# Kernel tuning notes

Measured on AMD Instinct MI355X. Metric: run time of the kernel, lower is better.

The kernel has to match this reference:

```python
import jax, jax.numpy as jnp
import numpy as np

B, T, C = 4, 2048, 1024
H = 16
D = C // H  # head_dim = 64


def setup_inputs() -> dict:
    key = jax.random.key(0)
    k1, k2, k3, k4, k5 = jax.random.split(key, 5)
    s = 1.0 / np.sqrt(C)
    return {
        "x": jax.random.normal(k1, (B, T, C), dtype=jnp.float32),
        "Wqkv": jax.random.normal(k2, (C, 3 * C), dtype=jnp.float32) * s,
        "bqkv": jax.random.normal(k3, (3 * C,), dtype=jnp.float32) * 0.02,
        "Wproj": jax.random.normal(k4, (C, C), dtype=jnp.float32) * s,
        "bproj": jax.random.normal(k5, (C,), dtype=jnp.float32) * 0.02,
    }


def reference(x, Wqkv, bqkv, Wproj, bproj):
    b, t, c = x.shape
    qkv = x @ Wqkv + bqkv                      # [B,T,3C]
    qkv = qkv.reshape(b, t, 3, H, D)
    q, k, v = (qkv[:, :, i].transpose(0, 2, 1, 3) for i in range(3))  # [B,H,T,D]
    scale = D ** -0.5
    attn = jnp.einsum("bhqd,bhkd->bhqk", q, k) * scale
    causal = jnp.tril(jnp.ones((t, t), dtype=bool))
    attn = jnp.where(causal[None, None], attn, -jnp.inf)
    attn = jax.nn.softmax(attn, axis=-1)
    out = jnp.einsum("bhqk,bhkd->bhqd", attn, v)  # [B,H,T,D]
    out = out.transpose(0, 2, 1, 3).reshape(b, t, c)
    return out @ Wproj + bproj
```

## Files before the change

### kernel.cpp

```cpp
#include <hip/hip_runtime.h>
#include <hip/hip_bf16.h>

typedef __bf16 bf16;
typedef __bf16 bf16x4 __attribute__((ext_vector_type(4)));
typedef __bf16 bf16x8 __attribute__((ext_vector_type(8)));
typedef float  f32x4  __attribute__((ext_vector_type(4)));

#define DEV static __device__ __forceinline__

static constexpr int Bsz = 4, T = 2048, C = 1024, H = 16;
static constexpr int M  = Bsz * T;
static constexpr int N1 = 3 * C;
static constexpr float SM_SCALE = 0.125f;

DEV void gload16(const bf16* g, const bf16* l) {
  __builtin_amdgcn_global_load_lds(
      (const __attribute__((address_space(1))) void*)g,
      (__attribute__((address_space(3))) void*)l, 16, 0, 0);
}

__launch_bounds__(256)
__global__ void convert_kernel(const float* __restrict__ in, bf16* __restrict__ out) {
  const size_t i = ((size_t)blockIdx.x * 256 + threadIdx.x) * 8;
  f32x4 a = *(const f32x4*)(in + i);
  f32x4 b = *(const f32x4*)(in + i + 4);
  *(bf16x4*)(out + i)     = __builtin_convertvector(a, bf16x4);
  *(bf16x4*)(out + i + 4) = __builtin_convertvector(b, bf16x4);
}

__launch_bounds__(256)
__global__ void transpose_conv_kernel(const float* __restrict__ in,
                                      bf16* __restrict__ out, int K, int N) {
  __shared__ float t[32][33];
  const int n0 = blockIdx.x * 32, k0 = blockIdx.y * 32;
  const int tx = threadIdx.x & 31, ty = threadIdx.x >> 5;
#pragma unroll
  for (int j = 0; j < 4; ++j)
    t[ty + j * 8][tx] = in[(size_t)(k0 + ty + j * 8) * N + n0 + tx];
  __syncthreads();
#pragma unroll
  for (int j = 0; j < 4; ++j)
    out[(size_t)(n0 + ty + j * 8) * K + k0 + tx] = (bf16)t[tx][ty + j * 8];
}

template <bool OUT_BF16, bool V_SPLIT>
__launch_bounds__(256)
__global__ void gemm_kernel(const bf16* __restrict__ A,
                            const bf16* __restrict__ Bt,
                            const float* __restrict__ bias,
                            void* __restrict__ Out, bf16* __restrict__ vt,
                            int Ndim, int Kdim) {
  __shared__ bf16 lds_a[128 * 64];
  __shared__ bf16 lds_b[128 * 64];
  const int tid = threadIdx.x;
  const int l = tid & 63, wid = tid >> 6;
  const int wm = wid >> 1, wn = wid & 1;
  const int lr = l & 15, lh = l >> 4;
  const int gx = gridDim.x, cpx = gx >> 3;
  const int L = blockIdx.y * gx + blockIdx.x;
  const int xcd = L & 7, q = L >> 3;
  const int m0 = (xcd * cpx + (q & (cpx - 1))) * 128;
  const int n0 = (q / cpx) * 128;
  const int r8 = l >> 3, g8 = (l & 7) * 8;

  f32x4 acc[4][4] = {};

  for (int k0 = 0; k0 < Kdim; k0 += 64) {
    __syncthreads();
#pragma unroll
    for (int i = 0; i < 4; ++i) {
      const int c = wid * 4 + i;
      const int row = c * 8 + r8;
      gload16(A  + (size_t)(m0 + row) * Kdim + k0 + g8, &lds_a[c * 512]);
      gload16(Bt + (size_t)(n0 + row) * Kdim + k0 + g8, &lds_b[c * 512]);
    }
    __syncthreads();
#pragma unroll
    for (int kk = 0; kk < 2; ++kk) {
      bf16x8 af[4], bfr[4];
#pragma unroll
      for (int mi = 0; mi < 4; ++mi)
        af[mi] = *(const bf16x8*)&lds_a[(wm * 64 + mi * 16 + lr) * 64 + kk * 32 + lh * 8];
#pragma unroll
      for (int ni = 0; ni < 4; ++ni)
        bfr[ni] = *(const bf16x8*)&lds_b[(wn * 64 + ni * 16 + lr) * 64 + kk * 32 + lh * 8];
#pragma unroll
      for (int mi = 0; mi < 4; ++mi)
#pragma unroll
        for (int ni = 0; ni < 4; ++ni)
          acc[mi][ni] = __builtin_amdgcn_mfma_f32_16x16x32_bf16(
              af[mi], bfr[ni], acc[mi][ni], 0, 0, 0);
    }
  }
  if (V_SPLIT && n0 >= 2 * C) {
    const int b = m0 >> 11, tb = (m0 & 2047) + wm * 64;
#pragma unroll
    for (int ni = 0; ni < 4; ++ni) {
      const int col = n0 - 2 * C + wn * 64 + ni * 16 + lr;
      const int hh = col >> 6, dd = col & 63;
      const float bv = bias[2 * C + col];
      bf16* vdst = vt + ((size_t)((b * H + hh) * 64 + dd)) * T + tb + lh * 4;
#pragma unroll
      for (int mi = 0; mi < 4; ++mi) {
        bf16x4 p4;
#pragma unroll
        for (int r = 0; r < 4; ++r) p4[r] = (bf16)(acc[mi][ni][r] + bv);
        *(bf16x4*)&vdst[mi * 16] = p4;
      }
    }
  } else {
#pragma unroll
    for (int ni = 0; ni < 4; ++ni) {
      const int col = n0 + wn * 64 + ni * 16 + lr;
      const float bv = bias[col];
#pragma unroll
      for (int mi = 0; mi < 4; ++mi) {
#pragma unroll
        for (int r = 0; r < 4; ++r) {
          const int row = m0 + wm * 64 + mi * 16 + lh * 4 + r;
          const float v = acc[mi][ni][r] + bv;
          if (OUT_BF16)
            ((bf16*)Out)[(size_t)row * Ndim + col] = (bf16)v;
          else
            ((float*)Out)[(size_t)row * Ndim + col] = v;
        }
      }
    }
  }
}

DEV int vswz(int d, int key) {
  return (d * 64 + key) ^ ((((d & 7) ^ (d >> 3)) & 7) << 3);
}

__launch_bounds__(256)
__global__ void attn_kernel(const bf16* __restrict__ qk,
                            const bf16* __restrict__ vt,
                            bf16* __restrict__ out) {
  __shared__ bf16 lds_k[2][64 * 64];
  __shared__ bf16 lds_vt[2][64 * 64];
  __shared__ bf16 lds_p[4][16 * 64];
  const int tid = threadIdx.x, l = tid & 63, w = tid >> 6;
  const int lr = l & 15, lh = l >> 4;
  const int p = blockIdx.x;
  const int bh = p >> 4, jj = p & 15;
  const int b = bh >> 4, h = bh & 15;
  const size_t RS = 2 * C;
  const bf16* base  = qk + (size_t)b * T * RS;
  const bf16* kbase = base + C + h * 64;
  const bf16* vth   = vt + (size_t)bh * 64 * T;
  bf16* op = out + (size_t)b * T * C + h * 64;
  const int r1 = tid >> 3, cc = tid & 7;
  const int kc = cc ^ (r1 & 7);

  for (int it = 0; it < 2; ++it) {
    const int qt = it ? jj : 31 - jj;
    const int q16 = qt * 64 + w * 16;
    bf16x8 qf[2];
#pragma unroll
    for (int kk = 0; kk < 2; ++kk) {
      bf16x8 qv = *(const bf16x8*)(base + (size_t)(q16 + lr) * RS + h * 64 + kk * 32 + lh * 8);
#pragma unroll
      for (int j = 0; j < 8; ++j) qf[kk][j] = (bf16)((float)qv[j] * SM_SCALE);
    }

    float mq = -__builtin_inff(), lq = 0.f;
    f32x4 o[4] = {};

    __syncthreads();
#pragma unroll
    for (int i = 0; i < 2; ++i) {
      const int row = i * 32 + r1;
      gload16(kbase + (size_t)row * RS + kc * 8, &lds_k[0][i * 2048 + w * 512]);
      const int vc = cc ^ (((r1 & 7) ^ (i * 4 + (r1 >> 3))) & 7);
      gload16(vth + (size_t)row * T + vc * 8, &lds_vt[0][i * 2048 + w * 512]);
    }
    __syncthreads();

    int buf = 0;
    for (int kt = 0; kt <= qt; ++kt) {
      const bf16* kb = &lds_k[buf][0];
      const bf16* vb = &lds_vt[buf][0];
      if (kt < qt) {
        const int nb = buf ^ 1;
#pragma unroll
        for (int i = 0; i < 2; ++i) {
          const int row = i * 32 + r1;
          gload16(kbase + (size_t)((kt + 1) * 64 + row) * RS + kc * 8,
                  &lds_k[nb][i * 2048 + w * 512]);
          const int vc = cc ^ (((r1 & 7) ^ (i * 4 + (r1 >> 3))) & 7);
          gload16(vth + (size_t)row * T + (kt + 1) * 64 + vc * 8,
                  &lds_vt[nb][i * 2048 + w * 512]);
        }
      }

      f32x4 s4[4] = {};
      __builtin_amdgcn_s_setprio(1);
#pragma unroll
      for (int kk = 0; kk < 2; ++kk) {
#pragma unroll
        for (int kn = 0; kn < 4; ++kn) {
          const int key = kn * 16 + lr;
          bf16x8 kf = *(const bf16x8*)&kb[(key * 64 + kk * 32 + lh * 8) ^ ((key & 7) << 3)];
          s4[kn] = __builtin_amdgcn_mfma_f32_16x16x32_bf16(kf, qf[kk], s4[kn], 0, 0, 0);
        }
      }
      __builtin_amdgcn_s_setprio(0);
      if (kt == qt) {
        const int qloc = w * 16 + lr;
#pragma unroll
        for (int kn = 0; kn < 4; ++kn)
#pragma unroll
          for (int r = 0; r < 4; ++r)
            if ((kn * 16 + lh * 4 + r) > qloc) s4[kn][r] = -__builtin_inff();
      }
      float pm = s4[0][0];
#pragma unroll
      for (int kn = 0; kn < 4; ++kn)
#pragma unroll
        for (int r = 0; r < 4; ++r) pm = fmaxf(pm, s4[kn][r]);
      pm = fmaxf(pm, __shfl_xor(pm, 16));
      pm = fmaxf(pm, __shfl_xor(pm, 32));
      const float mnew = fmaxf(mq, pm);
      const float alpha_q = __expf(mq - mnew);
      mq = mnew;
      float ssum = 0.f;
#pragma unroll
      for (int kn = 0; kn < 4; ++kn)
#pragma unroll
        for (int r = 0; r < 4; ++r) {
          const float p2 = __expf(s4[kn][r] - mnew);
          s4[kn][r] = p2;
          ssum += p2;
        }
#pragma unroll
      for (int kn = 0; kn < 4; ++kn) {
        bf16x4 pb;
#pragma unroll
        for (int r = 0; r < 4; ++r) pb[r] = (bf16)s4[kn][r];
        *(bf16x4*)&lds_p[w][(lr * 64 + kn * 16 + lh * 4) ^ ((lr & 7) << 3)] = pb;
      }
      ssum += __shfl_xor(ssum, 16);
      ssum += __shfl_xor(ssum, 32);
      lq = lq * alpha_q + ssum;
      float al[4];
#pragma unroll
      for (int r = 0; r < 4; ++r) al[r] = __shfl(alpha_q, lh * 4 + r);
#pragma unroll
      for (int ni = 0; ni < 4; ++ni)
#pragma unroll
        for (int r = 0; r < 4; ++r) o[ni][r] *= al[r];
      __builtin_amdgcn_s_setprio(1);
#pragma unroll
      for (int kk = 0; kk < 2; ++kk) {
        bf16x8 pf = *(const bf16x8*)&lds_p[w][(lr * 64 + kk * 32 + lh * 8) ^ ((lr & 7) << 3)];
#pragma unroll
        for (int ni = 0; ni < 4; ++ni) {
          const int d = ni * 16 + lr;
          bf16x8 vf = *(const bf16x8*)&vb[vswz(d, kk * 32 + lh * 8)];
          o[ni] = __builtin_amdgcn_mfma_f32_16x16x32_bf16(pf, vf, o[ni], 0, 0, 0);
        }
      }
      __builtin_amdgcn_s_setprio(0);

      if (kt < qt) {
        __syncthreads();
        buf ^= 1;
      }
    }
    float lrec[4];
#pragma unroll
    for (int r = 0; r < 4; ++r) lrec[r] = 1.0f / __shfl(lq, lh * 4 + r);
#pragma unroll
    for (int ni = 0; ni < 4; ++ni)
#pragma unroll
      for (int r = 0; r < 4; ++r) {
        const int qrow = q16 + lh * 4 + r;
        op[(size_t)qrow * C + ni * 16 + lr] = (bf16)(o[ni][r] * lrec[r]);
      }
  }
}

extern "C" void kernel_launch(void* const* d_in, const int* in_sizes, int n_in,
                              void* d_out, int out_size, void* d_ws, size_t ws_size,
                              hipStream_t stream) {
  const float* x     = (const float*)d_in[0];
  const float* Wqkv  = (const float*)d_in[1];
  const float* bqkv  = (const float*)d_in[2];
  const float* Wproj = (const float*)d_in[3];
  const float* bproj = (const float*)d_in[4];
  float* out = (float*)d_out;

  char* ws = (char*)d_ws;
  bf16* qk       = (bf16*)(ws);
  bf16* vt       = (bf16*)(ws + 33554432);
  bf16* wqkvt    = (bf16*)(ws + 50331648);
  bf16* wprojt   = (bf16*)(ws + 56623104);
  bf16* attn_out = (bf16*)(ws + 58720256);
  bf16* x_bf16   = attn_out;

  convert_kernel<<<dim3(M * C / (256 * 8)), 256, 0, stream>>>(x, x_bf16);
  transpose_conv_kernel<<<dim3(N1 / 32, C / 32), 256, 0, stream>>>(Wqkv, wqkvt, C, N1);
  transpose_conv_kernel<<<dim3(C / 32, C / 32), 256, 0, stream>>>(Wproj, wprojt, C, C);
  gemm_kernel<true, true><<<dim3(M / 128, N1 / 128), 256, 0, stream>>>(
      x_bf16, wqkvt, bqkv, qk, vt, 2 * C, C);
  attn_kernel<<<dim3(Bsz * H * 16), 256, 0, stream>>>(qk, vt, attn_out);
  gemm_kernel<false, false><<<dim3(M / 128, C / 128), 256, 0, stream>>>(
      attn_out, wprojt, bproj, out, nullptr, C, C);
}
```

Measured before the change: 307.7 us.

## Enlarge attention tiles to 128 queries and 128 keys with 512-thread blocks

```diff
diff --git a/kernel.cpp b/kernel.cpp
--- a/kernel.cpp
+++ b/kernel.cpp
@@ -56,11 +56,7 @@
   const int l = tid & 63, wid = tid >> 6;
   const int wm = wid >> 1, wn = wid & 1;
   const int lr = l & 15, lh = l >> 4;
-  const int gx = gridDim.x, cpx = gx >> 3;
-  const int L = blockIdx.y * gx + blockIdx.x;
-  const int xcd = L & 7, q = L >> 3;
-  const int m0 = (xcd * cpx + (q & (cpx - 1))) * 128;
-  const int n0 = (q / cpx) * 128;
+  const int m0 = blockIdx.x * 128, n0 = blockIdx.y * 128;
   const int r8 = l >> 3, g8 = (l & 7) * 8;
 
   f32x4 acc[4][4] = {};
@@ -129,21 +125,19 @@
   }
 }
 
-DEV int vswz(int d, int key) {
-  return (d * 64 + key) ^ ((((d & 7) ^ (d >> 3)) & 7) << 3);
-}
-
-__launch_bounds__(256)
+DEV int vswz3(int d) { return (d & 7) ^ ((d >> 3) & 7); }
+
+__launch_bounds__(512, 4)
 __global__ void attn_kernel(const bf16* __restrict__ qk,
                             const bf16* __restrict__ vt,
                             bf16* __restrict__ out) {
-  __shared__ bf16 lds_k[2][64 * 64];
-  __shared__ bf16 lds_vt[2][64 * 64];
-  __shared__ bf16 lds_p[4][16 * 64];
+  __shared__ bf16 lds_k[2][128 * 64];
+  __shared__ bf16 lds_vt[2][64 * 128];
+  __shared__ bf16 lds_p[8][16 * 64];
   const int tid = threadIdx.x, l = tid & 63, w = tid >> 6;
   const int lr = l & 15, lh = l >> 4;
   const int p = blockIdx.x;
-  const int bh = p >> 4, jj = p & 15;
+  const int bh = p >> 3, jj = p & 7;
   const int b = bh >> 4, h = bh & 15;
   const size_t RS = 2 * C;
   const bf16* base  = qk + (size_t)b * T * RS;
@@ -152,10 +146,24 @@
   bf16* op = out + (size_t)b * T * C + h * 64;
   const int r1 = tid >> 3, cc = tid & 7;
   const int kc = cc ^ (r1 & 7);
+  const int dV = tid >> 4, cV = tid & 15;
+
+  auto STAGE = [&](int nb, int kt) {
+#pragma unroll
+    for (int i = 0; i < 2; ++i) {
+      const int rowK = i * 64 + r1;
+      gload16(kbase + (size_t)(kt * 128 + rowK) * RS + kc * 8,
+              &lds_k[nb][i * 4096 + w * 512]);
+      const int d = i * 32 + dV;
+      const int vc = (cV & 8) | (((cV & 7) ^ vswz3(d)) & 7);
+      gload16(vth + (size_t)d * T + kt * 128 + vc * 8,
+              &lds_vt[nb][i * 4096 + w * 512]);
+    }
+  };
 
   for (int it = 0; it < 2; ++it) {
-    const int qt = it ? jj : 31 - jj;
-    const int q16 = qt * 64 + w * 16;
+    const int J = it ? jj : 15 - jj;
+    const int q16 = J * 128 + w * 16;
     bf16x8 qf[2];
 #pragma unroll
     for (int kk = 0; kk < 2; ++kk) {
@@ -168,57 +176,40 @@
     f32x4 o[4] = {};
 
     __syncthreads();
-#pragma unroll
-    for (int i = 0; i < 2; ++i) {
-      const int row = i * 32 + r1;
-      gload16(kbase + (size_t)row * RS + kc * 8, &lds_k[0][i * 2048 + w * 512]);
-      const int vc = cc ^ (((r1 & 7) ^ (i * 4 + (r1 >> 3))) & 7);
-      gload16(vth + (size_t)row * T + vc * 8, &lds_vt[0][i * 2048 + w * 512]);
-    }
+    STAGE(0, 0);
     __syncthreads();
 
     int buf = 0;
-    for (int kt = 0; kt <= qt; ++kt) {
+    for (int kt = 0; kt <= J; ++kt) {
       const bf16* kb = &lds_k[buf][0];
       const bf16* vb = &lds_vt[buf][0];
-      if (kt < qt) {
-        const int nb = buf ^ 1;
-#pragma unroll
-        for (int i = 0; i < 2; ++i) {
-          const int row = i * 32 + r1;
-          gload16(kbase + (size_t)((kt + 1) * 64 + row) * RS + kc * 8,
-                  &lds_k[nb][i * 2048 + w * 512]);
-          const int vc = cc ^ (((r1 & 7) ^ (i * 4 + (r1 >> 3))) & 7);
-          gload16(vth + (size_t)row * T + (kt + 1) * 64 + vc * 8,
-                  &lds_vt[nb][i * 2048 + w * 512]);
-        }
-      }
-
-      f32x4 s4[4] = {};
+      if (kt < J) STAGE(buf ^ 1, kt + 1);
+
+      f32x4 s8[8] = {};
       __builtin_amdgcn_s_setprio(1);
 #pragma unroll
       for (int kk = 0; kk < 2; ++kk) {
 #pragma unroll
-        for (int kn = 0; kn < 4; ++kn) {
+        for (int kn = 0; kn < 8; ++kn) {
           const int key = kn * 16 + lr;
           bf16x8 kf = *(const bf16x8*)&kb[(key * 64 + kk * 32 + lh * 8) ^ ((key & 7) << 3)];
-          s4[kn] = __builtin_amdgcn_mfma_f32_16x16x32_bf16(kf, qf[kk], s4[kn], 0, 0, 0);
+          s8[kn] = __builtin_amdgcn_mfma_f32_16x16x32_bf16(kf, qf[kk], s8[kn], 0, 0, 0);
         }
       }
       __builtin_amdgcn_s_setprio(0);
-      if (kt == qt) {
+      if (kt == J) {
         const int qloc = w * 16 + lr;
 #pragma unroll
-        for (int kn = 0; kn < 4; ++kn)
+        for (int kn = 0; kn < 8; ++kn)
 #pragma unroll
           for (int r = 0; r < 4; ++r)
-            if ((kn * 16 + lh * 4 + r) > qloc) s4[kn][r] = -__builtin_inff();
-      }
-      float pm = s4[0][0];
-#pragma unroll
-      for (int kn = 0; kn < 4; ++kn)
-#pragma unroll
-        for (int r = 0; r < 4; ++r) pm = fmaxf(pm, s4[kn][r]);
+            if ((kn * 16 + lh * 4 + r) > qloc) s8[kn][r] = -__builtin_inff();
+      }
+      float pm = s8[0][0];
+#pragma unroll
+      for (int kn = 0; kn < 8; ++kn)
+#pragma unroll
+        for (int r = 0; r < 4; ++r) pm = fmaxf(pm, s8[kn][r]);
       pm = fmaxf(pm, __shfl_xor(pm, 16));
       pm = fmaxf(pm, __shfl_xor(pm, 32));
       const float mnew = fmaxf(mq, pm);
@@ -226,20 +217,13 @@
       mq = mnew;
       float ssum = 0.f;
 #pragma unroll
-      for (int kn = 0; kn < 4; ++kn)
+      for (int kn = 0; kn < 8; ++kn)
 #pragma unroll
         for (int r = 0; r < 4; ++r) {
-          const float p2 = __expf(s4[kn][r] - mnew);
-          s4[kn][r] = p2;
+          const float p2 = __expf(s8[kn][r] - mnew);
+          s8[kn][r] = p2;
           ssum += p2;
         }
-#pragma unroll
-      for (int kn = 0; kn < 4; ++kn) {
-        bf16x4 pb;
-#pragma unroll
-        for (int r = 0; r < 4; ++r) pb[r] = (bf16)s4[kn][r];
-        *(bf16x4*)&lds_p[w][(lr * 64 + kn * 16 + lh * 4) ^ ((lr & 7) << 3)] = pb;
-      }
       ssum += __shfl_xor(ssum, 16);
       ssum += __shfl_xor(ssum, 32);
       lq = lq * alpha_q + ssum;
@@ -250,20 +234,32 @@
       for (int ni = 0; ni < 4; ++ni)
 #pragma unroll
         for (int r = 0; r < 4; ++r) o[ni][r] *= al[r];
-      __builtin_amdgcn_s_setprio(1);
-#pragma unroll
-      for (int kk = 0; kk < 2; ++kk) {
-        bf16x8 pf = *(const bf16x8*)&lds_p[w][(lr * 64 + kk * 32 + lh * 8) ^ ((lr & 7) << 3)];
-#pragma unroll
-        for (int ni = 0; ni < 4; ++ni) {
-          const int d = ni * 16 + lr;
-          bf16x8 vf = *(const bf16x8*)&vb[vswz(d, kk * 32 + lh * 8)];
-          o[ni] = __builtin_amdgcn_mfma_f32_16x16x32_bf16(pf, vf, o[ni], 0, 0, 0);
-        }
-      }
-      __builtin_amdgcn_s_setprio(0);
-
-      if (kt < qt) {
+#pragma unroll
+      for (int hh = 0; hh < 2; ++hh) {
+#pragma unroll
+        for (int kn4 = 0; kn4 < 4; ++kn4) {
+          const int kn = hh * 4 + kn4;
+          bf16x4 pb;
+#pragma unroll
+          for (int r = 0; r < 4; ++r) pb[r] = (bf16)s8[kn][r];
+          *(bf16x4*)&lds_p[w][(lr * 64 + kn4 * 16 + lh * 4) ^ ((lr & 7) << 3)] = pb;
+        }
+        __builtin_amdgcn_s_setprio(1);
+#pragma unroll
+        for (int kkl = 0; kkl < 2; ++kkl) {
+          bf16x8 pf = *(const bf16x8*)&lds_p[w][(lr * 64 + kkl * 32 + lh * 8) ^ ((lr & 7) << 3)];
+#pragma unroll
+          for (int ni = 0; ni < 4; ++ni) {
+            const int d = ni * 16 + lr;
+            const int key = hh * 64 + kkl * 32 + lh * 8;
+            bf16x8 vf = *(const bf16x8*)&vb[d * 128 + (key ^ (vswz3(d) << 3))];
+            o[ni] = __builtin_amdgcn_mfma_f32_16x16x32_bf16(pf, vf, o[ni], 0, 0, 0);
+          }
+        }
+        __builtin_amdgcn_s_setprio(0);
+      }
+
+      if (kt < J) {
         __syncthreads();
         buf ^= 1;
       }
@@ -304,7 +300,7 @@
   transpose_conv_kernel<<<dim3(C / 32, C / 32), 256, 0, stream>>>(Wproj, wprojt, C, C);
   gemm_kernel<true, true><<<dim3(M / 128, N1 / 128), 256, 0, stream>>>(
       x_bf16, wqkvt, bqkv, qk, vt, 2 * C, C);
-  attn_kernel<<<dim3(Bsz * H * 16), 256, 0, stream>>>(qk, vt, attn_out);
+  attn_kernel<<<dim3(Bsz * H * 8), 512, 0, stream>>>(qk, vt, attn_out);
   gemm_kernel<false, false><<<dim3(M / 128, C / 128), 256, 0, stream>>>(
       attn_out, wprojt, bproj, out, nullptr, C, C);
 }
```

After: 291.9 us. 5.1% less time.
